# Kernel tuning notes

Hardware: AMD Instinct MI355X
Metric: run time of the kernel (lower is better)

The kernel has to match this reference:

```python
import jax, jax.numpy as jnp
import numpy as np

B, Q, KV = 8, 16, 2048
NQ, NK, NV, H = 512, 512, 512, 512

def setup_inputs() -> dict:
    key = jax.random.key(0)
    k = jax.random.split(key, 7)
    s = 0.02
    return {
        "query": jax.random.normal(k[0], (B, Q, NQ), jnp.float32),
        "keys": jax.random.normal(k[1], (B, KV, NK), jnp.float32),
        "values": jax.random.normal(k[2], (B, KV, NV), jnp.float32),
        "W_weight": jax.random.normal(k[3], (H, NQ + NK), jnp.float32) * s,
        "W_bias": jax.random.normal(k[4], (H,), jnp.float32) * s,
        "v_weight": jax.random.normal(k[5], (1, H), jnp.float32) * s,
        "v_bias": jax.random.normal(k[6], (1,), jnp.float32) * s,
    }

def reference(query, keys, values, W_weight, W_bias, v_weight, v_bias):
    # Split W over the concat axis: cat([query, keys]) @ W^T == query@Wq^T + keys@Wk^T
    Wq = W_weight[:, :NQ]   # [H, Nq]
    Wk = W_weight[:, NQ:]   # [H, Nk]
    q_part = jnp.einsum('bqn,hn->bqh', query, Wq)   # [B,Q,H]
    k_part = jnp.einsum('bkn,hn->bkh', keys, Wk)    # [B,KV,H]
    # broadcast-add -> [B,KV,Q,H], tanh, project to scalar energy
    energy = jnp.tanh(k_part[:, :, None, :] + q_part[:, None, :, :] + W_bias)
    e = jnp.einsum('bkqh,h->bkq', energy, v_weight[0]) + v_bias[0]  # [B,KV,Q]
    scores = jax.nn.softmax(e, axis=1)              # softmax over KV
    # output = (values^T @ scores)^T -> [B,Q,Nv]
    output = jnp.einsum('bkn,bkq->bqn', values, scores)
    return output
```

## Files before the change

kernel.cpp:

```cpp
#include <hip/hip_runtime.h>
#include <cstddef>

using bf16x8  = __attribute__((ext_vector_type(8))) short;
using short4v = __attribute__((ext_vector_type(4))) short;
using f32x4   = __attribute__((ext_vector_type(4))) float;
using ushort8 = __attribute__((ext_vector_type(8))) unsigned short;

#define GLL16(gp, lp) __builtin_amdgcn_global_load_lds( \
    (const __attribute__((address_space(1))) unsigned int*)(const void*)(gp), \
    (__attribute__((address_space(3))) unsigned int*)(void*)(lp), 16, 0, 0)

__device__ __forceinline__ float exp2_f(float x){ float r; asm("v_exp_f32 %0, %1" : "=v"(r) : "v"(x)); return r; }
__device__ __forceinline__ float rcp_f (float x){ float r; asm("v_rcp_f32 %0, %1" : "=v"(r) : "v"(x)); return r; }
__device__ __forceinline__ unsigned pk2(float lo, float hi){
  unsigned r; asm("v_cvt_pk_bf16_f32 %0, %1, %2" : "=v"(r) : "v"(lo), "v"(hi)); return r;
}
__device__ __forceinline__ unsigned short f2bf(float f){
  unsigned int u = __float_as_uint(f);
  u = u + 0x7FFFu + ((u >> 16) & 1u);
  return (unsigned short)(u >> 16);
}
__device__ __forceinline__ float bf2f(unsigned short s){
  return __uint_as_float(((unsigned int)s) << 16);
}

#define QUAD(E, k0v,k1v,k2v,k3v, w0v,w1v,w2v,w3v, a) { \
  const float d0 = fmaf((k0v), (E).x, 1.f); \
  const float d1 = fmaf((k1v), (E).y, 1.f); \
  const float d2 = fmaf((k2v), (E).z, 1.f); \
  const float d3 = fmaf((k3v), (E).w, 1.f); \
  const float p01 = d0 * d1, p23 = d2 * d3; \
  const float n01 = fmaf((w1v), d0, (w0v) * d1); \
  const float n23 = fmaf((w3v), d2, (w2v) * d3); \
  (a) = fmaf(fmaf(n01, p23, n23 * p01), rcp_f(p01 * p23), (a)); }

#define KEYS_N   8388608
#define QG_BLOCKS 16
#define CONV_BLOCKS 4224
#define SCALE_2LOG2E 2.885390081777927f

#define OFF_KEYS_BF   0u
#define OFF_WK_BF     16777216u
#define OFF_EQB       17301504u
#define OFF_EPART     17563648u
#define OFF_SC        21757952u

__global__ __launch_bounds__(256) void k_convert(
    const float* __restrict__ keys, const float* __restrict__ W,
    const float* __restrict__ query,
    unsigned short* __restrict__ keys_bf, unsigned short* __restrict__ wk_bf,
    float* __restrict__ eqb)
{
  __shared__ short qg[128*32 + 32*32];
  if (blockIdx.x < QG_BLOCKS) {
    const int n0 = blockIdx.x * 32;
    const int tid = threadIdx.x;
    const int l = tid & 63, w = tid >> 6;
    short* A  = qg;
    short* Bs = qg + 4096;
    const int sub = tid >> 3;
    const int c4  = (tid & 7) * 4;
    const int wm = w & 1, wn = w >> 1;
    const int fr = l & 15, fg = l >> 4;

    f32x4 acc[4];
    #pragma unroll
    for (int i = 0; i < 4; ++i) acc[i] = (f32x4){0.f,0.f,0.f,0.f};

    float4 a4[4], b4, a4n[4], b4n;
    #pragma unroll
    for (int m = 0; m < 4; ++m)
      a4[m] = *(const float4*)(query + (size_t)(m * 32 + sub) * 512 + c4);
    b4 = *(const float4*)(W + (size_t)(n0 + sub) * 1024 + c4);

    for (int kt = 0; kt < 16; ++kt) {
      if (kt < 15) {
        const int k0 = (kt + 1) * 32;
        #pragma unroll
        for (int m = 0; m < 4; ++m)
          a4n[m] = *(const float4*)(query + (size_t)(m * 32 + sub) * 512 + k0 + c4);
        b4n = *(const float4*)(W + (size_t)(n0 + sub) * 1024 + k0 + c4);
      }
      __syncthreads();
      #pragma unroll
      for (int m = 0; m < 4; ++m) {
        const int row = m * 32 + sub;
        const int o = row * 32 + (((c4 >> 3) ^ ((row >> 1) & 3)) << 3) + (c4 & 7);
        *(uint2*)&A[o] = make_uint2(pk2(a4[m].x, a4[m].y), pk2(a4[m].z, a4[m].w));
      }
      {
        const int o = sub * 32 + (((c4 >> 3) ^ ((sub >> 1) & 3)) << 3) + (c4 & 7);
        *(uint2*)&Bs[o] = make_uint2(pk2(b4.x, b4.y), pk2(b4.z, b4.w));
      }
      __syncthreads();
      bf16x8 af[4], bfv;
      #pragma unroll
      for (int i = 0; i < 4; ++i) {
        const int ar = wm*64 + i*16 + fr;
        af[i] = *(const bf16x8*)&A[ar*32 + ((fg ^ ((ar>>1)&3)) << 3)];
      }
      const int br = wn*16 + fr;
      bfv = *(const bf16x8*)&Bs[br*32 + ((fg ^ ((br>>1)&3)) << 3)];
      #pragma unroll
      for (int i = 0; i < 4; ++i)
        acc[i] = __builtin_amdgcn_mfma_f32_16x16x32_bf16(af[i], bfv, acc[i], 0, 0, 0);
      if (kt < 15) {
        #pragma unroll
        for (int m = 0; m < 4; ++m) a4[m] = a4n[m];
        b4 = b4n;
      }
    }
    const int gh = n0 + wn*16 + fr;
    #pragma unroll
    for (int i = 0; i < 4; ++i)
      #pragma unroll
      for (int r = 0; r < 4; ++r) {
        const int gm = wm*64 + i*16 + fg*4 + r;
        eqb[gm * 512 + gh] = exp2_f(acc[i][r] * SCALE_2LOG2E);
      }
    return;
  }
  int idx = ((blockIdx.x - QG_BLOCKS) * 256 + threadIdx.x) * 8;
  const float* src;
  unsigned short* dst;
  if (idx < KEYS_N) { src = keys + idx; dst = keys_bf + idx; }
  else {
    int e = idx - KEYS_N;
    src = W + (size_t)(e >> 9) * 1024 + 512 + (e & 511);
    dst = wk_bf + e;
  }
  float4 a = *(const float4*)src;
  float4 b = *(const float4*)(src + 4);
  ushort8 o;
  o[0]=f2bf(a.x); o[1]=f2bf(a.y); o[2]=f2bf(a.z); o[3]=f2bf(a.w);
  o[4]=f2bf(b.x); o[5]=f2bf(b.y); o[6]=f2bf(b.z); o[7]=f2bf(b.w);
  *(ushort8*)dst = o;
}

struct FusedSM {
  union {
    struct { short A[2][8192]; short B[2][8192]; } g;
    unsigned short ekbf[128 * 128];
  } u;
  float eqs[16 * 128];
};

__global__ __launch_bounds__(256, 2) void k_fused(
    const unsigned short* __restrict__ keys_bf, const unsigned short* __restrict__ wk_bf,
    const float* __restrict__ w_bias, const float* __restrict__ eqb,
    const float* __restrict__ vw, float* __restrict__ e_part)
{
  __shared__ FusedSM sm;
  const int tid = threadIdx.x;
  const int l = tid & 63, w = tid >> 6;
  const int by = blockIdx.x;
  const int hc = blockIdx.y;
  const int h0 = hc * 128;
  const int b  = by >> 4;

  {
    const int q = tid >> 4, c0 = (tid & 15) * 8;
    const float* src = eqb + (size_t)(b * 16 + q) * 512 + h0 + c0;
    *(float4*)&sm.eqs[q * 128 + c0]     = *(const float4*)src;
    *(float4*)&sm.eqs[q * 128 + c0 + 4] = *(const float4*)(src + 4);
  }

  const unsigned short* Aptr = keys_bf + (size_t)by * 128 * 512;
  const unsigned short* Bptr = wk_bf + (size_t)h0 * 512;

  const int srow = w * 32 + (l >> 3);
  const int scol = ((l & 7) ^ (l >> 3)) * 8;
  const int wm = w >> 1, wn = w & 1;
  const int fr = l & 15, fg = l >> 4;
  const int axk = fr & 7;

  f32x4 acc[4][4];
  #pragma unroll
  for (int i = 0; i < 4; ++i)
    #pragma unroll
    for (int j = 0; j < 4; ++j) acc[i][j] = (f32x4){0.f,0.f,0.f,0.f};

  auto stage = [&](int buf, int kt) {
    const int k0 = kt * 64;
    #pragma unroll
    for (int r = 0; r < 4; ++r) {
      GLL16(Aptr + (srow + r * 8) * 512 + k0 + scol, &sm.u.g.A[buf][w * 2048 + r * 512]);
      GLL16(Bptr + (srow + r * 8) * 512 + k0 + scol, &sm.u.g.B[buf][w * 2048 + r * 512]);
    }
  };
  auto compute = [&](int buf) {
    #pragma unroll
    for (int ks = 0; ks < 2; ++ks) {
      bf16x8 af[4], bfv[4];
      #pragma unroll
      for (int i = 0; i < 4; ++i) {
        af[i]  = *(const bf16x8*)&sm.u.g.A[buf][(wm*64 + i*16 + fr) * 64 + ((ks*4 + fg) ^ axk) * 8];
        bfv[i] = *(const bf16x8*)&sm.u.g.B[buf][(wn*64 + i*16 + fr) * 64 + ((ks*4 + fg) ^ axk) * 8];
      }
      #pragma unroll
      for (int i = 0; i < 4; ++i)
        #pragma unroll
        for (int j = 0; j < 4; ++j)
          acc[i][j] = __builtin_amdgcn_mfma_f32_16x16x32_bf16(af[i], bfv[j], acc[i][j], 0, 0, 0);
    }
  };

  stage(0, 0);
  #pragma unroll 1
  for (int kt = 0; kt < 8; ++kt) {
    if (kt < 7) {
      stage((kt + 1) & 1, kt + 1);
      asm volatile("s_waitcnt vmcnt(8)" ::: "memory");
    } else {
      asm volatile("s_waitcnt vmcnt(0)" ::: "memory");
    }
    __builtin_amdgcn_sched_barrier(0);
    __builtin_amdgcn_s_barrier();
    __builtin_amdgcn_sched_barrier(0);
    compute(kt & 1);
    asm volatile("s_waitcnt lgkmcnt(0)" ::: "memory");
    __builtin_amdgcn_sched_barrier(0);
    __builtin_amdgcn_s_barrier();
    __builtin_amdgcn_sched_barrier(0);
  }

  #pragma unroll
  for (int j = 0; j < 4; ++j) {
    const int col = wn*64 + j*16 + fr;
    const float bias = w_bias[h0 + col];
    const int chunk = col >> 3, coff = col & 7;
    #pragma unroll
    for (int i = 0; i < 4; ++i)
      #pragma unroll
      for (int r = 0; r < 4; ++r) {
        const int row = wm*64 + i*16 + fg*4 + r;
        const float ev = exp2_f((acc[i][j][r] + bias) * SCALE_2LOG2E);
        sm.u.ekbf[row * 128 + ((chunk ^ (fg*4 + r)) << 3) + coff] = f2bf(ev);
      }
  }
  const int g = l & 3, kl = l >> 2;
  float vv[32];
  #pragma unroll
  for (int s = 0; s < 4; ++s) {
    const float4 a0 = *(const float4*)(vw + h0 + s*32 + g*4);
    const float4 a1 = *(const float4*)(vw + h0 + s*32 + 16 + g*4);
    vv[s*8+0]=-2.f*a0.x; vv[s*8+1]=-2.f*a0.y; vv[s*8+2]=-2.f*a0.z; vv[s*8+3]=-2.f*a0.w;
    vv[s*8+4]=-2.f*a1.x; vv[s*8+5]=-2.f*a1.y; vv[s*8+6]=-2.f*a1.z; vv[s*8+7]=-2.f*a1.w;
  }
  __syncthreads();

  {
    const int lr0 = w * 32 + kl;
    const int lr1 = lr0 + 16;
    float ek0[32], ek1[32];
    #pragma unroll
    for (int s = 0; s < 4; ++s)
      #pragma unroll
      for (int hf = 0; hf < 2; ++hf) {
        const int ck = (4*s + 2*hf + (g >> 1)) ^ kl;
        const short4v v40 = *(const short4v*)&sm.u.ekbf[lr0 * 128 + (ck << 3) + (g & 1) * 4];
        const short4v v41 = *(const short4v*)&sm.u.ekbf[lr1 * 128 + (ck << 3) + (g & 1) * 4];
        #pragma unroll
        for (int u = 0; u < 4; ++u) {
          ek0[s*8 + hf*4 + u] = bf2f((unsigned short)v40[u]);
          ek1[s*8 + hf*4 + u] = bf2f((unsigned short)v41[u]);
        }
      }
    const size_t ep0 = (size_t)hc * 262144 + ((size_t)(by * 128 + lr0)) * 16;
    const size_t ep1 = (size_t)hc * 262144 + ((size_t)(by * 128 + lr1)) * 16;
    #pragma unroll 4
    for (int q = 0; q < 16; ++q) {
      float a00 = 0.f, a01 = 0.f, a10 = 0.f, a11 = 0.f;
      #pragma unroll
      for (int s = 0; s < 4; ++s) {
        const float* er = &sm.eqs[q * 128 + s * 32 + g * 4];
        const float4 E0 = *(const float4*)er;
        const float4 E1 = *(const float4*)(er + 16);
        QUAD(E0, ek0[s*8+0],ek0[s*8+1],ek0[s*8+2],ek0[s*8+3],
                 vv[s*8+0],vv[s*8+1],vv[s*8+2],vv[s*8+3], a00);
        QUAD(E1, ek0[s*8+4],ek0[s*8+5],ek0[s*8+6],ek0[s*8+7],
                 vv[s*8+4],vv[s*8+5],vv[s*8+6],vv[s*8+7], a01);
        QUAD(E0, ek1[s*8+0],ek1[s*8+1],ek1[s*8+2],ek1[s*8+3],
                 vv[s*8+0],vv[s*8+1],vv[s*8+2],vv[s*8+3], a10);
        QUAD(E1, ek1[s*8+4],ek1[s*8+5],ek1[s*8+6],ek1[s*8+7],
                 vv[s*8+4],vv[s*8+5],vv[s*8+6],vv[s*8+7], a11);
      }
      float r0 = a00 + a01;
      r0 += __shfl_xor(r0, 1, 64);
      r0 += __shfl_xor(r0, 2, 64);
      float r1 = a10 + a11;
      r1 += __shfl_xor(r1, 1, 64);
      r1 += __shfl_xor(r1, 2, 64);
      if (g == 0) { e_part[ep0 + q] = r0; e_part[ep1 + q] = r1; }
    }
  }
}

__global__ __launch_bounds__(256) void k_softmax(
    const float* __restrict__ e_part, float* __restrict__ sc)
{
  const int b = blockIdx.x >> 4, q = blockIdx.x & 15;
  const int base = b * 32768 + q;
  const int tid = threadIdx.x;
  __shared__ float redm[4], reds[4];

  float vals[8];
  float mx = -1e30f;
  #pragma unroll
  for (int i = 0; i < 8; ++i) {
    const int x = base + (tid + i * 256) * 16;
    vals[i] = (e_part[x] + e_part[x + 262144]) + (e_part[x + 524288] + e_part[x + 786432]);
    mx = fmaxf(mx, vals[i]);
  }
  #pragma unroll
  for (int msk = 1; msk < 64; msk <<= 1) mx = fmaxf(mx, __shfl_xor(mx, msk, 64));
  if ((tid & 63) == 0) redm[tid >> 6] = mx;
  __syncthreads();
  mx = fmaxf(fmaxf(redm[0], redm[1]), fmaxf(redm[2], redm[3]));

  float ex[8], sum = 0.f;
  #pragma unroll
  for (int i = 0; i < 8; ++i) { ex[i] = __expf(vals[i] - mx); sum += ex[i]; }
  #pragma unroll
  for (int msk = 1; msk < 64; msk <<= 1) sum += __shfl_xor(sum, msk, 64);
  if ((tid & 63) == 0) reds[tid >> 6] = sum;
  __syncthreads();
  sum = reds[0] + reds[1] + reds[2] + reds[3];
  const float r = 1.f / sum;
  #pragma unroll
  for (int i = 0; i < 8; ++i) sc[base + (tid + i * 256) * 16] = ex[i] * r;
}

__global__ __launch_bounds__(512) void k_pv(
    const float* __restrict__ values, const float* __restrict__ sc,
    float* __restrict__ out)
{
  __shared__ float lds[128 * 20];
  const int tid = threadIdx.x;
  const int nc = blockIdx.x & 31, b = blockIdx.x >> 5;
  const int n = tid & 15, kg = tid >> 4;
  const int l = tid & 63, w = tid >> 6;
  const int n0 = nc * 16;

  float acc[16];
  #pragma unroll
  for (int q = 0; q < 16; ++q) acc[q] = 0.f;

  for (int kc = 0; kc < 16; ++kc) {
    __syncthreads();
    {
      const float* ssrc = sc + (size_t)(b * 2048 + kc * 128) * 16;
      const int row = tid >> 2, c4 = (tid & 3) * 4;
      *(float4*)&lds[row * 20 + c4] = *(const float4*)&ssrc[row * 16 + c4];
    }
    __syncthreads();
    const float* vb = values + ((size_t)(b * 2048 + kc * 128 + kg * 4)) * 512 + n0 + n;
    #pragma unroll
    for (int k2 = 0; k2 < 4; ++k2) {
      const float v = vb[(size_t)k2 * 512];
      const float* sr = &lds[(kg * 4 + k2) * 20];
      #pragma unroll
      for (int qq = 0; qq < 4; ++qq) {
        const float4 s4 = *(const float4*)&sr[qq * 4];
        acc[qq*4+0] = fmaf(v, s4.x, acc[qq*4+0]);
        acc[qq*4+1] = fmaf(v, s4.y, acc[qq*4+1]);
        acc[qq*4+2] = fmaf(v, s4.z, acc[qq*4+2]);
        acc[qq*4+3] = fmaf(v, s4.w, acc[qq*4+3]);
      }
    }
  }
  #pragma unroll
  for (int q = 0; q < 16; ++q) {
    acc[q] += __shfl_xor(acc[q], 16, 64);
    acc[q] += __shfl_xor(acc[q], 32, 64);
  }
  __syncthreads();
  if (l < 16) {
    #pragma unroll
    for (int q = 0; q < 16; ++q) lds[w * 256 + q * 16 + l] = acc[q];
  }
  __syncthreads();
  if (tid < 256) {
    const int q = tid >> 4, nn = tid & 15;
    float s = 0.f;
    #pragma unroll
    for (int w2 = 0; w2 < 8; ++w2) s += lds[w2 * 256 + q * 16 + nn];
    out[((size_t)(b * 16 + q)) * 512 + n0 + nn] = s;
  }
}

extern "C" void kernel_launch(void* const* d_in, const int* in_sizes, int n_in,
                              void* d_out, int out_size, void* d_ws, size_t ws_size,
                              hipStream_t stream)
{
  const float* query  = (const float*)d_in[0];
  const float* keys   = (const float*)d_in[1];
  const float* values = (const float*)d_in[2];
  const float* W      = (const float*)d_in[3];
  const float* w_bias = (const float*)d_in[4];
  const float* vw     = (const float*)d_in[5];

  char* ws = (char*)d_ws;
  unsigned short* keys_bf = (unsigned short*)(ws + OFF_KEYS_BF);
  unsigned short* wk_bf   = (unsigned short*)(ws + OFF_WK_BF);
  float* eqb    = (float*)(ws + OFF_EQB);
  float* e_part = (float*)(ws + OFF_EPART);
  float* sc     = (float*)(ws + OFF_SC);

  hipLaunchKernelGGL(k_convert, dim3(QG_BLOCKS + CONV_BLOCKS), dim3(256), 0, stream,
                     keys, W, query, keys_bf, wk_bf, eqb);
  hipLaunchKernelGGL(k_fused, dim3(128, 4), dim3(256), 0, stream,
                     keys_bf, wk_bf, w_bias, eqb, vw, e_part);
  hipLaunchKernelGGL(k_softmax, dim3(128), dim3(256), 0, stream, e_part, sc);
  hipLaunchKernelGGL(k_pv, dim3(256), dim3(512), 0, stream, values, sc, (float*)d_out);
}
```

Measured before the change: 83.74 us.

## Fuse keys fp32-to-bf16 conversion into the GEMM tile loader

Removes the separate bulk conversion of keys to bf16 (and its 16MB workspace round trip). The fused kernel now loads fp32 keys into registers, packs them to bf16 and writes them into swizzled LDS, while Wk still uses direct global-to-LDS loads. The K-loop pipeline is reordered so the next A tile is prefetched into registers during compute. This cuts global traffic but costs extra registers and VALU work in the fused kernel, and each keys tile is now read once per H-chunk (4x) in fp32.

```diff
diff --git a/kernel.cpp b/kernel.cpp
--- a/kernel.cpp
+++ b/kernel.cpp
@@ -34,22 +34,18 @@
   const float n23 = fmaf((w3v), d2, (w2v) * d3); \
   (a) = fmaf(fmaf(n01, p23, n23 * p01), rcp_f(p01 * p23), (a)); }
 
-#define KEYS_N   8388608
 #define QG_BLOCKS 16
-#define CONV_BLOCKS 4224
+#define WK_BLOCKS 128
 #define SCALE_2LOG2E 2.885390081777927f
 
-#define OFF_KEYS_BF   0u
-#define OFF_WK_BF     16777216u
-#define OFF_EQB       17301504u
-#define OFF_EPART     17563648u
-#define OFF_SC        21757952u
+#define OFF_WK_BF     0u
+#define OFF_EQB       524288u
+#define OFF_EPART     786432u
+#define OFF_SC        4980736u
 
 __global__ __launch_bounds__(256) void k_convert(
-    const float* __restrict__ keys, const float* __restrict__ W,
-    const float* __restrict__ query,
-    unsigned short* __restrict__ keys_bf, unsigned short* __restrict__ wk_bf,
-    float* __restrict__ eqb)
+    const float* __restrict__ W, const float* __restrict__ query,
+    unsigned short* __restrict__ wk_bf, float* __restrict__ eqb)
 {
   __shared__ short qg[128*32 + 32*32];
   if (blockIdx.x < QG_BLOCKS) {
@@ -120,21 +116,14 @@
       }
     return;
   }
-  int idx = ((blockIdx.x - QG_BLOCKS) * 256 + threadIdx.x) * 8;
-  const float* src;
-  unsigned short* dst;
-  if (idx < KEYS_N) { src = keys + idx; dst = keys_bf + idx; }
-  else {
-    int e = idx - KEYS_N;
-    src = W + (size_t)(e >> 9) * 1024 + 512 + (e & 511);
-    dst = wk_bf + e;
-  }
+  int e = (blockIdx.x - QG_BLOCKS) * 2048 + threadIdx.x * 8;
+  const float* src = W + (size_t)(e >> 9) * 1024 + 512 + (e & 511);
   float4 a = *(const float4*)src;
   float4 b = *(const float4*)(src + 4);
   ushort8 o;
   o[0]=f2bf(a.x); o[1]=f2bf(a.y); o[2]=f2bf(a.z); o[3]=f2bf(a.w);
   o[4]=f2bf(b.x); o[5]=f2bf(b.y); o[6]=f2bf(b.z); o[7]=f2bf(b.w);
-  *(ushort8*)dst = o;
+  *(ushort8*)&wk_bf[e] = o;
 }
 
 struct FusedSM {
@@ -146,7 +135,7 @@
 };
 
 __global__ __launch_bounds__(256, 2) void k_fused(
-    const unsigned short* __restrict__ keys_bf, const unsigned short* __restrict__ wk_bf,
+    const float* __restrict__ keys, const unsigned short* __restrict__ wk_bf,
     const float* __restrict__ w_bias, const float* __restrict__ eqb,
     const float* __restrict__ vw, float* __restrict__ e_part)
 {
@@ -164,8 +153,9 @@
     *(float4*)&sm.eqs[q * 128 + c0]     = *(const float4*)src;
     *(float4*)&sm.eqs[q * 128 + c0 + 4] = *(const float4*)(src + 4);
   }
-
-  const unsigned short* Aptr = keys_bf + (size_t)by * 128 * 512;
+  asm volatile("s_waitcnt vmcnt(0)" ::: "memory");
+
+  const float* Akeys = keys + (size_t)by * 128 * 512;
   const unsigned short* Bptr = wk_bf + (size_t)h0 * 512;
 
   const int srow = w * 32 + (l >> 3);
@@ -180,13 +170,30 @@
     #pragma unroll
     for (int j = 0; j < 4; ++j) acc[i][j] = (f32x4){0.f,0.f,0.f,0.f};
 
-  auto stage = [&](int buf, int kt) {
+  float4 areg[8];
+  auto aload = [&](int kt) {
+    const float* src = Akeys + kt * 64;
+    #pragma unroll
+    for (int m = 0; m < 8; ++m) {
+      const int u = m * 256 + tid;
+      areg[m] = *(const float4*)(src + (size_t)(u >> 4) * 512 + (u & 15) * 4);
+    }
+  };
+  auto awrite = [&](int buf) {
+    #pragma unroll
+    for (int m = 0; m < 8; ++m) {
+      const int u = m * 256 + tid;
+      const int row = u >> 4, c4 = u & 15;
+      const int o = row * 64 + (((c4 >> 1) ^ (row & 7)) << 3) + (c4 & 1) * 4;
+      *(uint2*)&sm.u.g.A[buf][o] =
+          make_uint2(pk2(areg[m].x, areg[m].y), pk2(areg[m].z, areg[m].w));
+    }
+  };
+  auto bstage = [&](int buf, int kt) {
     const int k0 = kt * 64;
     #pragma unroll
-    for (int r = 0; r < 4; ++r) {
-      GLL16(Aptr + (srow + r * 8) * 512 + k0 + scol, &sm.u.g.A[buf][w * 2048 + r * 512]);
+    for (int r = 0; r < 4; ++r)
       GLL16(Bptr + (srow + r * 8) * 512 + k0 + scol, &sm.u.g.B[buf][w * 2048 + r * 512]);
-    }
   };
   auto compute = [&](int buf) {
     #pragma unroll
@@ -205,24 +212,35 @@
     }
   };
 
-  stage(0, 0);
+  aload(0);
+  asm volatile("s_waitcnt vmcnt(0)" ::: "memory");
+  awrite(0);
+  bstage(0, 0);
+
   #pragma unroll 1
   for (int kt = 0; kt < 8; ++kt) {
     if (kt < 7) {
-      stage((kt + 1) & 1, kt + 1);
+      aload(kt + 1);
       asm volatile("s_waitcnt vmcnt(8)" ::: "memory");
     } else {
       asm volatile("s_waitcnt vmcnt(0)" ::: "memory");
     }
-    __builtin_amdgcn_sched_barrier(0);
-    __builtin_amdgcn_s_barrier();
-    __builtin_amdgcn_sched_barrier(0);
-    compute(kt & 1);
     asm volatile("s_waitcnt lgkmcnt(0)" ::: "memory");
     __builtin_amdgcn_sched_barrier(0);
     __builtin_amdgcn_s_barrier();
     __builtin_amdgcn_sched_barrier(0);
-  }
+    if (kt < 7) bstage((kt + 1) & 1, kt + 1);
+    compute(kt & 1);
+    if (kt < 7) {
+      asm volatile("s_waitcnt vmcnt(4)" ::: "memory");
+      __builtin_amdgcn_sched_barrier(0);
+      awrite((kt + 1) & 1);
+    }
+  }
+  asm volatile("s_waitcnt lgkmcnt(0)" ::: "memory");
+  __builtin_amdgcn_sched_barrier(0);
+  __builtin_amdgcn_s_barrier();
+  __builtin_amdgcn_sched_barrier(0);
 
   #pragma unroll
   for (int j = 0; j < 4; ++j) {
@@ -401,16 +419,15 @@
   const float* vw     = (const float*)d_in[5];
 
   char* ws = (char*)d_ws;
-  unsigned short* keys_bf = (unsigned short*)(ws + OFF_KEYS_BF);
-  unsigned short* wk_bf   = (unsigned short*)(ws + OFF_WK_BF);
+  unsigned short* wk_bf = (unsigned short*)(ws + OFF_WK_BF);
   float* eqb    = (float*)(ws + OFF_EQB);
   float* e_part = (float*)(ws + OFF_EPART);
   float* sc     = (float*)(ws + OFF_SC);
 
-  hipLaunchKernelGGL(k_convert, dim3(QG_BLOCKS + CONV_BLOCKS), dim3(256), 0, stream,
-                     keys, W, query, keys_bf, wk_bf, eqb);
+  hipLaunchKernelGGL(k_convert, dim3(QG_BLOCKS + WK_BLOCKS), dim3(256), 0, stream,
+                     W, query, wk_bf, eqb);
   hipLaunchKernelGGL(k_fused, dim3(128, 4), dim3(256), 0, stream,
-                     keys_bf, wk_bf, w_bias, eqb, vw, e_part);
+                     keys, wk_bf, w_bias, eqb, vw, e_part);
   hipLaunchKernelGGL(k_softmax, dim3(128), dim3(256), 0, stream, e_part, sc);
   hipLaunchKernelGGL(k_pv, dim3(256), dim3(512), 0, stream, values, sc, (float*)d_out);
 }
```

New measurement: 82.88 us. No clear change (-1.0%).
